# Optimization experiments

Hardware: AMD Instinct MI355X
Metric: run time of the kernel (lower is better)

## Reference

```python
import jax, jax.numpy as jnp
import numpy as np


def setup_inputs() -> dict:
    key = jax.random.key(0)
    k1, k2, k3 = jax.random.split(key, 3)
    B, H, W = 4, 1024, 1024
    GD, GH, GW = 8, 16, 16
    NIN, NOUT = 3, 3
    grid = jax.random.normal(k1, (B, (NIN + 1) * NOUT, GD, GH, GW), dtype=jnp.float32)
    guide = jax.random.uniform(k2, (B, 1, H, W), dtype=jnp.float32)  # in [0,1)
    image = jax.random.uniform(k3, (B, NIN, H, W), dtype=jnp.float32)
    return {"grid": grid, "guide": guide, "image": image}


def _bilateral_slice_apply(grid, guide, image):
    """HDRNet bilateral slice + per-pixel affine apply.

    grid:  [B, (n_in+1)*n_out, gd, gh, gw]
    guide: [B, 1, H, W], values in [0, 1]
    image: [B, n_in, H, W]
    out:   [B, n_out, H, W]
    """
    B, C, GD, GH, GW = grid.shape
    _, NIN, H, W = image.shape
    NOUT = C // (NIN + 1)

    # Continuous grid coordinates (HDRNet convention: sample at pixel centers,
    # shifted by -0.5 so tent weights are centered on grid cells).
    gx = (jnp.arange(W, dtype=jnp.float32) + 0.5) * (GW / W) - 0.5  # [W]
    gy = (jnp.arange(H, dtype=jnp.float32) + 0.5) * (GH / H) - 0.5  # [H]
    gz = guide[:, 0] * GD - 0.5                                      # [B,H,W]

    fx, fy, fz = jnp.floor(gx), jnp.floor(gy), jnp.floor(gz)

    def gather_corner(g, zi, yi, xi):
        # g: [C,gd,gh,gw]; zi: [H,W]; yi: [H]; xi: [W] -> [C,H,W]
        return g[:, zi, yi[:, None], xi[None, :]]

    gather_b = jax.vmap(gather_corner, in_axes=(0, 0, None, None))

    acc = jnp.zeros((B, C, H, W), dtype=grid.dtype)
    for dz in (0.0, 1.0):
        zf = fz + dz
        wz = jnp.maximum(1.0 - jnp.abs(zf - gz), 0.0)               # [B,H,W]
        zi = jnp.clip(zf, 0, GD - 1).astype(jnp.int32)
        for dy in (0.0, 1.0):
            yf = fy + dy
            wy = jnp.maximum(1.0 - jnp.abs(yf - gy), 0.0)           # [H]
            yi = jnp.clip(yf, 0, GH - 1).astype(jnp.int32)
            for dx in (0.0, 1.0):
                xf = fx + dx
                wx = jnp.maximum(1.0 - jnp.abs(xf - gx), 0.0)       # [W]
                xi = jnp.clip(xf, 0, GW - 1).astype(jnp.int32)
                w = wz * (wy[:, None] * wx[None, :])                # [B,H,W]
                corner = gather_b(grid, zi, yi, xi)                 # [B,C,H,W]
                acc = acc + w[:, None] * corner

    # Per-pixel affine: out[o] = sum_j A[o,j] * in[j] + A[o,n_in]
    coeffs = acc.reshape(B, NOUT, NIN + 1, H, W)
    out = jnp.einsum('bojhw,bjhw->bohw', coeffs[:, :, :NIN], image) + coeffs[:, :, NIN]
    return out


def reference(grid, guide, image):
    return _bilateral_slice_apply(grid, guide, image)
```

## Files before the change

### kernel.cpp

```cpp
#include <hip/hip_runtime.h>
#include <hip/hip_fp16.h>

#define BATCH 4
#define HH 1024
#define WW 1024
#define GDp 8
#define NC 12
#define PAIR2 12
#define HROW2 268
#define NTILE 4

union V4 { int4 i4; __half2 h[4]; };
typedef float f4 __attribute__((ext_vector_type(4)));

__global__ __launch_bounds__(256, 4) void bsa_kernel(
    const float* __restrict__ grid,
    const float* __restrict__ guide,
    const float* __restrict__ image,
    float* __restrict__ out)
{
    __shared__ float sg[GDp][3][3][NC];
    __shared__ __align__(16) __half2 Hs2[2][16][HROW2];

    const int bx  = blockIdx.x;
    const int byc = blockIdx.y;
    const int b   = blockIdx.z;
    const int tx = threadIdx.x;
    const int ty = threadIdx.y;
    const int tid = ty * 16 + tx;
    const int lane = tid & 63;
    const int wv   = tid >> 6;

    const int x0  = bx * 64;
    const int y0c = byc * 64;
    const float inv64 = 1.0f / 64.0f;

    const float gy0c = (y0c + 0.5f) * inv64 - 0.5f;
    const int ylo = (int)floorf(gy0c);

    const int xloc = 4 * tx;
    const size_t plane = (size_t)HH * WW;
    const size_t gpix0 = ((size_t)(b * HH + y0c + ty)) * WW + x0 + xloc;
    const size_t ib0   = (size_t)b * 3 * plane + (size_t)(y0c + ty) * WW + x0 + xloc;

    f4 cg  = *(const f4*)&guide[gpix0];
    f4 ci0 = *(const f4*)&image[ib0];
    f4 ci1 = *(const f4*)&image[ib0 + plane];
    f4 ci2 = *(const f4*)&image[ib0 + 2 * plane];

    {
        const int z = tid >> 5;
        const int u = tid & 31;
        if (u < 27) {
            const int cell = (u * 11) >> 5;
            const int cq   = u - cell * 3;
            const int yy   = (cell * 11) >> 5;
            const int xx   = cell - yy * 3;
            const int gxi = min(max(bx - 1 + xx, 0), 15);
            const int gyi = min(max(ylo + yy, 0), 15);
            const float* gp = grid + (size_t)b * (NC * GDp * 256)
                                   + ((size_t)z * 16 + gyi) * 16 + gxi;
#pragma unroll
            for (int j = 0; j < 4; ++j) {
                const int c = cq * 4 + j;
                const int pos = (c < 8) ? ((c & 3) * 2 + (c >> 2)) : c;
                sg[z][yy][xx][pos] = gp[(size_t)c * (GDp * 256)];
            }
        }
    }
    __syncthreads();

    auto build_hs = [&](int buf, int t) {
        for (int u = lane; u < 96; u += 64) {
            const int rl   = (u * 171) >> 12;
            const int cell = u - rl * 24;
            const int r    = wv * 4 + rl;
            const int xs   = cell >> 3;
            const int z    = cell & 7;
            const float gy  = (y0c + t * 16 + r + 0.5f) * inv64 - 0.5f;
            const float fyf = floorf(gy);
            const float wy1 = gy - fyf;
            const float wy0 = 1.0f - wy1;
            const int ys0 = (int)fyf - ylo;
            const float* s0 = &sg[z][ys0][xs][0];
            const float* s1 = &sg[z][ys0 + 1][xs][0];
            __half2 h[6];
#pragma unroll
            for (int m = 0; m < 6; ++m) {
                h[m] = __floats2half2_rn(wy0 * s0[2*m]   + wy1 * s1[2*m],
                                         wy0 * s0[2*m+1] + wy1 * s1[2*m+1]);
            }
            __half2* rowp = &Hs2[buf][r][0];
            if (z < 7) {
                __half2* hd = rowp + (xs * 7 + z) * PAIR2;
#pragma unroll
                for (int m = 0; m < 6; ++m) hd[m] = h[m];
            }
            if (z > 0) {
                __half2* hd = rowp + (xs * 7 + (z - 1)) * PAIR2 + 6;
#pragma unroll
                for (int m = 0; m < 6; ++m) hd[m] = h[m];
            }
        }
    };

    build_hs(0, 0);

    const int xs0 = tx >> 3;
    const float fxf = (float)(bx - 1 + xs0);
    const float gxb = (x0 + xloc + 0.5f) * inv64 - 0.5f;
    const __half oneh = __float2half_rn(1.0f);

#pragma unroll
    for (int t = 0; t < NTILE; ++t) {
        f4 ng, ni0, ni1, ni2;
        if (t < NTILE - 1) {
            const size_t gp = gpix0 + (size_t)(t + 1) * 16 * WW;
            const size_t ip = ib0   + (size_t)(t + 1) * 16 * WW;
            ng  = *(const f4*)&guide[gp];
            ni0 = *(const f4*)&image[ip];
            ni1 = *(const f4*)&image[ip + plane];
            ni2 = *(const f4*)&image[ip + 2 * plane];
        }

        if (t < NTILE - 1) build_hs((t + 1) & 1, t + 1);

        const __half2* Hrow = &Hs2[t & 1][ty][0];
        const size_t ib = ib0 + (size_t)t * 16 * WW;

        const float gk[4]  = {cg.x, cg.y, cg.z, cg.w};
        const float ia[4]  = {ci0.x, ci0.y, ci0.z, ci0.w};
        const float ja[4]  = {ci1.x, ci1.y, ci1.z, ci1.w};
        const float ka[4]  = {ci2.x, ci2.y, ci2.z, ci2.w};
        float ok0[4], ok1[4], ok2[4];

#pragma unroll
        for (int k = 0; k < 4; ++k) {
            const float wx1 = (gxb - fxf) + (float)k * inv64;
            const float wx0 = 1.0f - wx1;

            const float gz  = fmaf(gk[k], 8.0f, -0.5f);
            const float fzf = floorf(gz);
            const float zpf = fminf(fmaxf(fzf, 0.0f), 6.0f);
            const float whi = fminf(fmaxf(gz - zpf, 0.0f), 1.0f);
            const float wlo = 1.0f - whi;
            const int zp = (int)zpf;

            const __half2 w00 = __float2half2_rn(wx0 * wlo);
            const __half2 w10 = __float2half2_rn(wx0 * whi);
            const __half2 w01 = __float2half2_rn(wx1 * wlo);
            const __half2 w11 = __float2half2_rn(wx1 * whi);

            const __half2* q = Hrow + (xs0 * 7 + zp) * PAIR2;
            V4 va, vb, vc, vd, ve, vf;
            va.i4 = *(const int4*)(q);
            vb.i4 = *(const int4*)(q + 4);
            vc.i4 = *(const int4*)(q + 8);
            vd.i4 = *(const int4*)(q + 7 * PAIR2);
            ve.i4 = *(const int4*)(q + 7 * PAIR2 + 4);
            vf.i4 = *(const int4*)(q + 7 * PAIR2 + 8);

            const __half2 A0 = va.h[0], A1 = va.h[1], A2 = va.h[2], A3 = va.h[3];
            const __half2 A4 = vb.h[0], A5 = vb.h[1];
            const __half2 B0 = vb.h[2], B1 = vb.h[3];
            const __half2 B2 = vc.h[0], B3 = vc.h[1], B4 = vc.h[2], B5 = vc.h[3];
            const __half2 C0 = vd.h[0], C1 = vd.h[1], C2 = vd.h[2], C3 = vd.h[3];
            const __half2 C4 = ve.h[0], C5 = ve.h[1];
            const __half2 D0 = ve.h[2], D1 = ve.h[3];
            const __half2 D2 = vf.h[0], D3 = vf.h[1], D4 = vf.h[2], D5 = vf.h[3];

            const __half2 r0 = __hfma2(w00, A0, __hfma2(w10, B0, __hfma2(w01, C0, __hmul2(w11, D0))));
            const __half2 r1 = __hfma2(w00, A1, __hfma2(w10, B1, __hfma2(w01, C1, __hmul2(w11, D1))));
            const __half2 r2 = __hfma2(w00, A2, __hfma2(w10, B2, __hfma2(w01, C2, __hmul2(w11, D2))));
            const __half2 r3 = __hfma2(w00, A3, __hfma2(w10, B3, __hfma2(w01, C3, __hmul2(w11, D3))));
            const __half2 r4 = __hfma2(w00, A4, __hfma2(w10, B4, __hfma2(w01, C4, __hmul2(w11, D4))));
            const __half2 r5 = __hfma2(w00, A5, __hfma2(w10, B5, __hfma2(w01, C5, __hmul2(w11, D5))));

            const __half i0h = __float2half_rn(ia[k]);
            const __half i1h = __float2half_rn(ja[k]);
            const __half i2h = __float2half_rn(ka[k]);
            const __half2 bi0 = __half2half2(i0h);
            const __half2 bi1 = __half2half2(i1h);
            const __half2 bi2 = __half2half2(i2h);

            const __half2 acc01 = __hfma2(bi0, r0, __hfma2(bi1, r1, __hfma2(bi2, r2, r3)));
            const __half2 d2 = __hfma2(__halves2half2(i0h, i1h), r4,
                                       __hmul2(__halves2half2(i2h, oneh), r5));

            ok0[k] = __low2float(acc01);
            ok1[k] = __high2float(acc01);
            ok2[k] = __half2float(__hadd(__low2half(d2), __high2half(d2)));
        }

        *(f4*)&out[ib]             = f4{ok0[0], ok0[1], ok0[2], ok0[3]};
        *(f4*)&out[ib + plane]     = f4{ok1[0], ok1[1], ok1[2], ok1[3]};
        *(f4*)&out[ib + 2 * plane] = f4{ok2[0], ok2[1], ok2[2], ok2[3]};

        if (t < NTILE - 1) { cg = ng; ci0 = ni0; ci1 = ni1; ci2 = ni2; }
    }
}

extern "C" void kernel_launch(void* const* d_in, const int* in_sizes, int n_in,
                              void* d_out, int out_size, void* d_ws, size_t ws_size,
                              hipStream_t stream) {
    const float* grid  = (const float*)d_in[0];
    const float* guide = (const float*)d_in[1];
    const float* image = (const float*)d_in[2];
    float* out = (float*)d_out;

    dim3 block(16, 16, 1);
    dim3 grid_dim(WW / 64, HH / 64, BATCH);
    bsa_kernel<<<grid_dim, block, 0, stream>>>(grid, guide, image, out);
}
```

Baseline: 24.75 us.

## Reshape block tile to 256x16 with one wavefront per row

Changes each block's tile from 64x64 pixels to 256 wide by 16 tall. Each wavefront now covers a full 256-pixel row segment with a float4 per lane, giving contiguous 1 KB row accesses. The shared grid slice grows to 6 x-cells, and the per-row half-precision table holds 4 rows per buffer instead of 16. This cuts shared memory and makes the table build one pass per wave, but the block loads more grid cells and the block count shifts shape.

```diff
diff --git a/kernel.cpp b/kernel.cpp
--- a/kernel.cpp
+++ b/kernel.cpp
@@ -7,7 +7,8 @@
 #define GDp 8
 #define NC 12
 #define PAIR2 12
-#define HROW2 268
+#define NXS 6
+#define HROW2 504
 #define NTILE 4
 
 union V4 { int4 i4; __half2 h[4]; };
@@ -19,65 +20,58 @@
     const float* __restrict__ image,
     float* __restrict__ out)
 {
-    __shared__ float sg[GDp][3][3][NC];
-    __shared__ __align__(16) __half2 Hs2[2][16][HROW2];
+    __shared__ float sg[GDp][3][NXS][NC];
+    __shared__ __align__(16) __half2 Hs2[2][4][HROW2];
 
     const int bx  = blockIdx.x;
     const int byc = blockIdx.y;
     const int b   = blockIdx.z;
-    const int tx = threadIdx.x;
-    const int ty = threadIdx.y;
-    const int tid = ty * 16 + tx;
+    const int tid  = threadIdx.y * 16 + threadIdx.x;
     const int lane = tid & 63;
     const int wv   = tid >> 6;
 
-    const int x0  = bx * 64;
-    const int y0c = byc * 64;
+    const int x0  = bx * 256;
+    const int y0c = byc * 16;
     const float inv64 = 1.0f / 64.0f;
 
     const float gy0c = (y0c + 0.5f) * inv64 - 0.5f;
     const int ylo = (int)floorf(gy0c);
 
-    const int xloc = 4 * tx;
+    const int xloc = 4 * lane;
     const size_t plane = (size_t)HH * WW;
-    const size_t gpix0 = ((size_t)(b * HH + y0c + ty)) * WW + x0 + xloc;
-    const size_t ib0   = (size_t)b * 3 * plane + (size_t)(y0c + ty) * WW + x0 + xloc;
+    const size_t gpix0 = ((size_t)(b * HH + y0c + wv)) * WW + x0 + xloc;
+    const size_t ib0   = (size_t)b * 3 * plane + (size_t)(y0c + wv) * WW + x0 + xloc;
 
     f4 cg  = *(const f4*)&guide[gpix0];
     f4 ci0 = *(const f4*)&image[ib0];
     f4 ci1 = *(const f4*)&image[ib0 + plane];
     f4 ci2 = *(const f4*)&image[ib0 + 2 * plane];
 
-    {
-        const int z = tid >> 5;
-        const int u = tid & 31;
-        if (u < 27) {
-            const int cell = (u * 11) >> 5;
-            const int cq   = u - cell * 3;
-            const int yy   = (cell * 11) >> 5;
-            const int xx   = cell - yy * 3;
-            const int gxi = min(max(bx - 1 + xx, 0), 15);
-            const int gyi = min(max(ylo + yy, 0), 15);
-            const float* gp = grid + (size_t)b * (NC * GDp * 256)
-                                   + ((size_t)z * 16 + gyi) * 16 + gxi;
-#pragma unroll
-            for (int j = 0; j < 4; ++j) {
-                const int c = cq * 4 + j;
-                const int pos = (c < 8) ? ((c & 3) * 2 + (c >> 2)) : c;
-                sg[z][yy][xx][pos] = gp[(size_t)c * (GDp * 256)];
-            }
+    for (int e = tid; e < 432; e += 256) {
+        const int z  = e / 54;
+        const int u  = e - z * 54;
+        const int cell = (u * 171) >> 9;
+        const int cq   = u - cell * 3;
+        const int yy   = (cell * 11) >> 6;
+        const int xx   = cell - yy * 6;
+        const int gxi = min(max(4 * bx - 1 + xx, 0), 15);
+        const int gyi = min(max(ylo + yy, 0), 15);
+        const float* gp = grid + (size_t)b * (NC * GDp * 256)
+                               + ((size_t)z * 16 + gyi) * 16 + gxi;
+#pragma unroll
+        for (int j = 0; j < 4; ++j) {
+            const int c = cq * 4 + j;
+            const int pos = (c < 8) ? ((c & 3) * 2 + (c >> 2)) : c;
+            sg[z][yy][xx][pos] = gp[(size_t)c * (GDp * 256)];
         }
     }
     __syncthreads();
 
     auto build_hs = [&](int buf, int t) {
-        for (int u = lane; u < 96; u += 64) {
-            const int rl   = (u * 171) >> 12;
-            const int cell = u - rl * 24;
-            const int r    = wv * 4 + rl;
-            const int xs   = cell >> 3;
-            const int z    = cell & 7;
-            const float gy  = (y0c + t * 16 + r + 0.5f) * inv64 - 0.5f;
+        if (lane < 48) {
+            const int xs = lane >> 3;
+            const int z  = lane & 7;
+            const float gy  = (y0c + t * 4 + wv + 0.5f) * inv64 - 0.5f;
             const float fyf = floorf(gy);
             const float wy1 = gy - fyf;
             const float wy0 = 1.0f - wy1;
@@ -90,7 +84,7 @@
                 h[m] = __floats2half2_rn(wy0 * s0[2*m]   + wy1 * s1[2*m],
                                          wy0 * s0[2*m+1] + wy1 * s1[2*m+1]);
             }
-            __half2* rowp = &Hs2[buf][r][0];
+            __half2* rowp = &Hs2[buf][wv][0];
             if (z < 7) {
                 __half2* hd = rowp + (xs * 7 + z) * PAIR2;
 #pragma unroll
@@ -106,8 +100,8 @@
 
     build_hs(0, 0);
 
-    const int xs0 = tx >> 3;
-    const float fxf = (float)(bx - 1 + xs0);
+    const int xs0 = (lane + 8) >> 4;
+    const float fxf = (float)(4 * bx - 1 + xs0);
     const float gxb = (x0 + xloc + 0.5f) * inv64 - 0.5f;
     const __half oneh = __float2half_rn(1.0f);
 
@@ -115,8 +109,8 @@
     for (int t = 0; t < NTILE; ++t) {
         f4 ng, ni0, ni1, ni2;
         if (t < NTILE - 1) {
-            const size_t gp = gpix0 + (size_t)(t + 1) * 16 * WW;
-            const size_t ip = ib0   + (size_t)(t + 1) * 16 * WW;
+            const size_t gp = gpix0 + (size_t)(t + 1) * 4 * WW;
+            const size_t ip = ib0   + (size_t)(t + 1) * 4 * WW;
             ng  = *(const f4*)&guide[gp];
             ni0 = *(const f4*)&image[ip];
             ni1 = *(const f4*)&image[ip + plane];
@@ -125,8 +119,8 @@
 
         if (t < NTILE - 1) build_hs((t + 1) & 1, t + 1);
 
-        const __half2* Hrow = &Hs2[t & 1][ty][0];
-        const size_t ib = ib0 + (size_t)t * 16 * WW;
+        const __half2* Hrow = &Hs2[t & 1][wv][0];
+        const size_t ib = ib0 + (size_t)t * 4 * WW;
 
         const float gk[4]  = {cg.x, cg.y, cg.z, cg.w};
         const float ia[4]  = {ci0.x, ci0.y, ci0.z, ci0.w};
@@ -209,6 +203,6 @@
     float* out = (float*)d_out;
 
     dim3 block(16, 16, 1);
-    dim3 grid_dim(WW / 64, HH / 64, BATCH);
+    dim3 grid_dim(WW / 256, HH / 16, BATCH);
     bsa_kernel<<<grid_dim, block, 0, stream>>>(grid, guide, image, out);
 }
```

Result: no change. 24.34 us (-1.6%).
